# Kernel tuning notes

Hardware: AMD Instinct MI355X
Metric: run time of the kernel (lower is better)

## Reference

```python
import jax, jax.numpy as jnp
import numpy as np

N = 65536          # nodes
E = 1048576        # edges (avg degree 16)
K = 5              # B-spline kernel size per dim (dim=3 -> 125 kernels)
F_IN, F_OUT = 1, 32
GRID = 32          # first sparse_voxel_max_pool: size = 1/32 -> 32^3 voxels
NUM_VOX = GRID ** 3

# enumerate the 2^3 corners of the degree-1 B-spline support
_BITS = np.array([[(b >> d) & 1 for d in range(3)] for b in range(8)], dtype=np.int32)  # [8,3]
_STRIDES = np.array([1, K, K * K], dtype=np.int32)  # kernel index strides per dim


def setup_inputs() -> dict:
    key = jax.random.key(0)
    ks = jax.random.split(key, 7)
    x = jax.random.normal(ks[0], (N, F_IN), dtype=jnp.float32)
    edge_index = jax.random.randint(ks[1], (2, E), 0, N, dtype=jnp.int32)
    pseudo = jax.random.uniform(ks[2], (E, 3), dtype=jnp.float32)   # edge pseudo-coords in [0,1]^3
    pos = jax.random.uniform(ks[3], (N, 3), dtype=jnp.float32)      # node positions in [0,1]^3
    W = jax.random.normal(ks[4], (K ** 3, F_IN, F_OUT), dtype=jnp.float32) * 0.1
    W_root = jax.random.normal(ks[5], (F_IN, F_OUT), dtype=jnp.float32) * 0.1
    bias = jax.random.normal(ks[6], (F_OUT,), dtype=jnp.float32) * 0.1
    return {"x": x, "edge_index": edge_index, "pseudo": pseudo, "pos": pos,
            "W": W, "W_root": W_root, "bias": bias}


def spline_basis(pseudo):
    """Degree-1 open B-spline basis. Returns (weights [E,8], kernel_idx [E,8])."""
    v = pseudo * (K - 1)                                   # [E,3] in [0, K-1]
    i0 = jnp.clip(jnp.floor(v), 0, K - 2)                  # lower knot per dim
    f = v - i0                                             # fractional part
    i0 = i0.astype(jnp.int32)
    bits = jnp.asarray(_BITS)                              # [8,3]
    idx = i0[:, None, :] + bits[None]                      # [E,8,3]
    w = jnp.where(bits[None].astype(bool), f[:, None, :], 1.0 - f[:, None, :])
    B = w.prod(axis=-1)                                    # [E,8]
    kidx = (idx * jnp.asarray(_STRIDES)).sum(axis=-1)      # [E,8] in [0,125)
    return B, kidx


def spline_conv(x, edge_index, pseudo, W, W_root, bias):
    src, dst = edge_index[0], edge_index[1]
    B, kidx = spline_basis(pseudo)                         # [E,8], [E,8]
    xj = x[src]                                            # [E,F_IN] edge-wise gather
    Wg = W[kidx]                                           # [E,8,F_IN,F_OUT]
    msg = jnp.einsum('es,ef,esfo->eo', B, xj, Wg)          # basis-weighted messages [E,F_OUT]
    agg = jax.ops.segment_sum(msg, dst, num_segments=N)    # scatter-add
    deg = jax.ops.segment_sum(jnp.ones((E,), jnp.float32), dst, num_segments=N)
    out = agg / jnp.clip(deg, 1.0)[:, None] + x @ W_root + bias  # mean aggr + root + bias
    return out


def reference(x, edge_index, pseudo, pos, W, W_root, bias):
    h = jax.nn.elu(spline_conv(x, edge_index, pseudo, W, W_root, bias))  # [N,32]
    # sparse voxel max pooling: hash positions to a 32^3 grid, scatter-max features
    vid = jnp.clip(jnp.floor(pos * GRID), 0, GRID - 1).astype(jnp.int32)  # [N,3]
    vidx = vid[:, 0] + GRID * vid[:, 1] + GRID * GRID * vid[:, 2]         # [N]
    pooled = jax.ops.segment_max(h, vidx, num_segments=NUM_VOX)           # [32768,32]
    pooled = jnp.where(jnp.isfinite(pooled), pooled, 0.0)                 # empty voxels -> 0
    return pooled
```

## Files before the change

kernel.cpp:

```cpp
#include <hip/hip_runtime.h>
#include <math.h>

#define F_OUT     32
#define GRID_DIM  32
#define NUM_VOX   (GRID_DIM * GRID_DIM * GRID_DIM)

#define NPB   64
#define NBKT  1024
#define SEB   4096
#define SCS   127
#define FOCAP 2048

__device__ __forceinline__ unsigned int enc_f32(float f) {
    unsigned int u = __float_as_uint(f);
    return (u & 0x80000000u) ? ~u : (u | 0x80000000u);
}
__device__ __forceinline__ float dec_f32(unsigned int e) {
    return (e & 0x80000000u) ? __uint_as_float(e ^ 0x80000000u)
                             : __uint_as_float(~e);
}

__global__ __launch_bounds__(512) void sort_kernel(
    const int*   __restrict__ src,
    const int*   __restrict__ dst,
    const float* __restrict__ x,
    const float* __restrict__ pseudo,
    float4* __restrict__ payload,
    unsigned int* __restrict__ off_tab,
    int E)
{
    __shared__ unsigned int   sHist[NBKT];
    __shared__ unsigned int   sStart[NBKT];
    __shared__ unsigned int   sScan[512];
    __shared__ unsigned int   sPairE[SEB];
    __shared__ unsigned short sPairD[SEB];

    const int t   = threadIdx.x;
    const int blk = blockIdx.x;
    const int e0  = blk * SEB;

    for (int i = t; i < NBKT; i += 512) sHist[i] = 0;
    __syncthreads();

    unsigned short dloc[8];
    #pragma unroll
    for (int i = 0; i < 8; ++i) {
        int e = e0 + i * 512 + t;
        if (e < E) {
            int d = dst[e];
            dloc[i] = (unsigned short)d;
            atomicAdd(&sHist[d >> 6], 1u);
        } else dloc[i] = 0;
    }
    __syncthreads();

    unsigned int a0 = sHist[2 * t], a1 = sHist[2 * t + 1];
    sScan[t] = a0 + a1;
    __syncthreads();
    for (int ofs = 1; ofs < 512; ofs <<= 1) {
        unsigned int v = (t >= ofs) ? sScan[t - ofs] : 0u;
        __syncthreads();
        sScan[t] += v;
        __syncthreads();
    }
    unsigned int excl = sScan[t] - (a0 + a1);
    sStart[2 * t]     = excl;
    sStart[2 * t + 1] = excl + a0;
    __syncthreads();
    sHist[2 * t]     = excl;
    sHist[2 * t + 1] = excl + a0;
    __syncthreads();

    #pragma unroll
    for (int i = 0; i < 8; ++i) {
        int e = e0 + i * 512 + t;
        if (e < E) {
            unsigned int slot = atomicAdd(&sHist[dloc[i] >> 6], 1u);
            sPairE[slot] = (unsigned int)e;
            sPairD[slot] = dloc[i];
        }
    }
    __syncthreads();

    int total = E - e0; if (total > SEB) total = SEB;

    for (int i = t; i < total; i += 512) {
        unsigned int e = sPairE[i];
        unsigned int d = sPairD[i];
        float xj = x[src[e]];
        float p0 = pseudo[3 * e], p1 = pseudo[3 * e + 1], p2 = pseudo[3 * e + 2];
        unsigned int q2 = (unsigned int)(p2 * 65535.0f + 0.5f) & 0xFFFFu;
        unsigned int w  = q2 | ((d & 63u) << 16);
        payload[(size_t)e0 + i] = make_float4(p0, p1, xj, __uint_as_float(w));
    }

    for (int b = t; b < NBKT; b += 512)
        off_tab[(size_t)blk * (NBKT + 1) + b] = (unsigned int)e0 + sStart[b];
    if (t == 0)
        off_tab[(size_t)blk * (NBKT + 1) + NBKT] = (unsigned int)(e0 + total);
}

__global__ __launch_bounds__(512) void owner_kernel(
    const float4* __restrict__ payload,
    const unsigned int* __restrict__ off_tab,
    const float* __restrict__ W,
    const float* __restrict__ x,
    const float* __restrict__ W_root,
    const float* __restrict__ bias,
    const float* __restrict__ pos,
    unsigned int* __restrict__ pooled,
    int Nn, int nSB)
{
    __shared__ __align__(16) float sC[NPB * SCS];
    __shared__ unsigned int  sGS[256];
    __shared__ unsigned int  sLS[257];
    __shared__ unsigned int  sTmp[256];
    __shared__ unsigned char sFO[FOCAP];

    const int t = threadIdx.x;
    const int b = blockIdx.x;

    for (int i = t; i < NPB * SCS / 4; i += 512)
        *(float4*)&sC[i * 4] = make_float4(0.f, 0.f, 0.f, 0.f);

    unsigned int cnt = 0;
    if (t < 256) {
        if (t < nSB) {
            unsigned int s  = off_tab[(size_t)t * (NBKT + 1) + b];
            unsigned int e_ = off_tab[(size_t)t * (NBKT + 1) + b + 1];
            sGS[t] = s;
            cnt = e_ - s;
        } else sGS[t] = 0;
        sTmp[t] = cnt;
    }
    __syncthreads();
    for (int ofs = 1; ofs < 256; ofs <<= 1) {
        unsigned int v = 0;
        if (t < 256 && t >= ofs) v = sTmp[t - ofs];
        __syncthreads();
        if (t < 256) sTmp[t] += v;
        __syncthreads();
    }
    if (t < 256) sLS[t] = sTmp[t] - cnt;
    if (t == 255) sLS[256] = sTmp[255];
    __syncthreads();
    const int ne = (int)sLS[256];

    if (t < 256 && t < nSB) {
        unsigned int ls = sLS[t];
        for (unsigned int j = 0; j < cnt; ++j) {
            unsigned int idx = ls + j;
            if (idx < FOCAP) sFO[idx] = (unsigned char)t;
        }
    }
    __syncthreads();

    for (int i = t; i < ne; i += 512) {
        int f;
        if (i < FOCAP) f = sFO[i];
        else {
            int lo = 0, hi = 255;
            while (lo < hi) {
                int mid = (lo + hi + 1) >> 1;
                if (sLS[mid] <= (unsigned int)i) lo = mid; else hi = mid - 1;
            }
            f = lo;
        }
        unsigned int g = sGS[f] + ((unsigned int)i - sLS[f]);
        float4 r = payload[g];

        float xj = r.z;
        unsigned int w = __float_as_uint(r.w);
        int   rel = (int)((w >> 16) & 63u);
        float p2  = (float)(w & 0xFFFFu) * (1.0f / 65535.0f);

        float v0 = r.x * 4.0f, v1 = r.y * 4.0f, v2 = p2 * 4.0f;
        float i0 = fminf(fmaxf(floorf(v0), 0.0f), 3.0f);
        float i1 = fminf(fmaxf(floorf(v1), 0.0f), 3.0f);
        float i2 = fminf(fmaxf(floorf(v2), 0.0f), 3.0f);
        float f0 = v0 - i0, f1 = v1 - i1, f2 = v2 - i2;
        float g0 = 1.0f - f0, g1 = 1.0f - f1, g2 = 1.0f - f2;
        int k = (int)i0 + 5 * (int)i1 + 25 * (int)i2;

        float w00 = g0 * g1, w10 = f0 * g1, w01 = g0 * f1, w11 = f0 * f1;
        float a2 = xj * g2, b2 = xj * f2;
        float* row = sC + rel * SCS;
        atomicAdd(row + k +  0, w00 * a2);
        atomicAdd(row + k +  1, w10 * a2);
        atomicAdd(row + k +  5, w01 * a2);
        atomicAdd(row + k +  6, w11 * a2);
        atomicAdd(row + k + 25, w00 * b2);
        atomicAdd(row + k + 26, w10 * b2);
        atomicAdd(row + k + 30, w01 * b2);
        atomicAdd(row + k + 31, w11 * b2);
        atomicAdd(row + 125, 1.0f);
    }
    __syncthreads();

    const int node = t & 63;
    const int cg   = t >> 6;
    const float* crow = sC + node * SCS;
    float4 acc = make_float4(0.f, 0.f, 0.f, 0.f);
    #pragma unroll 5
    for (int k = 0; k < 125; ++k) {
        float r = crow[k];
        float4 wv = *(const float4*)(W + k * F_OUT + cg * 4);
        acc.x += r * wv.x; acc.y += r * wv.y;
        acc.z += r * wv.z; acc.w += r * wv.w;
    }
    float dg = fmaxf(crow[125], 1.0f);
    int   n  = b * NPB + node;
    float xn = (n < Nn) ? x[n] : 0.0f;
    float4 wr = *(const float4*)(W_root + cg * 4);
    float4 bs = *(const float4*)(bias + cg * 4);
    __syncthreads();

    if (n < Nn) {
        float h;
        h = acc.x / dg + xn * wr.x + bs.x; h = h > 0.f ? h : expm1f(h); sC[node * SCS + cg * 4 + 0] = h;
        h = acc.y / dg + xn * wr.y + bs.y; h = h > 0.f ? h : expm1f(h); sC[node * SCS + cg * 4 + 1] = h;
        h = acc.z / dg + xn * wr.z + bs.z; h = h > 0.f ? h : expm1f(h); sC[node * SCS + cg * 4 + 2] = h;
        h = acc.w / dg + xn * wr.w + bs.w; h = h > 0.f ? h : expm1f(h); sC[node * SCS + cg * 4 + 3] = h;
    }
    __syncthreads();

    for (int item = t; item < NPB * F_OUT; item += 512) {
        int nr = item >> 5, o = item & 31;
        int nn = b * NPB + nr;
        if (nn >= Nn) break;
        int vx = min(max((int)floorf(pos[3 * nn + 0] * (float)GRID_DIM), 0), GRID_DIM - 1);
        int vy = min(max((int)floorf(pos[3 * nn + 1] * (float)GRID_DIM), 0), GRID_DIM - 1);
        int vz = min(max((int)floorf(pos[3 * nn + 2] * (float)GRID_DIM), 0), GRID_DIM - 1);
        int vidx = vx + GRID_DIM * vy + GRID_DIM * GRID_DIM * vz;
        atomicMax(&pooled[(size_t)vidx * F_OUT + o], enc_f32(sC[nr * SCS + o]));
    }
}

__global__ __launch_bounds__(256) void finalize_kernel(
    const unsigned int* __restrict__ pooled,
    float* __restrict__ out, int M)
{
    int i = blockIdx.x * blockDim.x + threadIdx.x;
    if (i >= M) return;
    unsigned int u = pooled[i];
    out[i] = (u == 0u) ? 0.0f : dec_f32(u);
}

extern "C" void kernel_launch(void* const* d_in, const int* in_sizes, int n_in,
                              void* d_out, int out_size, void* d_ws, size_t ws_size,
                              hipStream_t stream) {
    const float* x       = (const float*)d_in[0];
    const int*   ei      = (const int*)  d_in[1];
    const float* pseudo  = (const float*)d_in[2];
    const float* pos     = (const float*)d_in[3];
    const float* W       = (const float*)d_in[4];
    const float* W_root  = (const float*)d_in[5];
    const float* bias    = (const float*)d_in[6];
    float* out = (float*)d_out;

    const int E   = in_sizes[1] / 2;
    const int Nn  = in_sizes[0];
    const int nSB = (E + SEB - 1) / SEB;
    const int nb  = (Nn + NPB - 1) / NPB;

    const size_t pooled_b = (size_t)NUM_VOX * F_OUT * 4;
    const size_t off_b    = (size_t)nSB * (NBKT + 1) * 4;
    unsigned int* pooled  = (unsigned int*)d_ws;
    unsigned int* off_tab = (unsigned int*)((char*)d_ws + pooled_b);
    float4*       payload = (float4*)((char*)d_ws + pooled_b + ((off_b + 15) & ~(size_t)15));

    hipMemsetAsync(pooled, 0, pooled_b, stream);

    sort_kernel<<<nSB, 512, 0, stream>>>(ei, ei + E, x, pseudo, payload, off_tab, E);
    owner_kernel<<<nb, 512, 0, stream>>>(payload, off_tab, W, x, W_root, bias, pos,
                                         pooled, Nn, nSB);

    const int M = (out_size < NUM_VOX * F_OUT) ? out_size : NUM_VOX * F_OUT;
    finalize_kernel<<<(M + 255) / 256, 256, 0, stream>>>(pooled, out, M);
}
```

Before: 173.3 us.

## Gather edge payload before bucketing and simplify owner-side edge indexing

The sort kernel now loads src, pseudo and x[src] in the first pass, before any sorting. It stages full float4 payloads in LDS and writes them out contiguously, which replaces the second scattered gather pass. The sort chunk size is halved so the LDS payload buffer fits. The offset table is packed as start|count per bucket. The owner kernel replaces its 256-wide block scan and segment lookup with a wave-shuffle scan plus an atomic base, building an LDS list of edge indices, with a direct-processing fallback when that list overflows. The W contraction is also vectorized over float4 rows. The trade-offs are twice as many sort blocks, twice as many segments per owner block, and a non-deterministic order of edge accumulation.

Result: faster. 167.3 us (-3.4%).

```diff
diff --git a/kernel.cpp b/kernel.cpp
--- a/kernel.cpp
+++ b/kernel.cpp
@@ -7,9 +7,10 @@
 
 #define NPB   64
 #define NBKT  1024
-#define SEB   4096
-#define SCS   127
-#define FOCAP 2048
+#define SEB   2048
+#define SCS   132
+#define DEGS  125
+#define ECAP  3072
 
 __device__ __forceinline__ unsigned int enc_f32(float f) {
     unsigned int u = __float_as_uint(f);
@@ -29,26 +30,31 @@
     unsigned int* __restrict__ off_tab,
     int E)
 {
-    __shared__ unsigned int   sHist[NBKT];
-    __shared__ unsigned int   sStart[NBKT];
-    __shared__ unsigned int   sScan[512];
-    __shared__ unsigned int   sPairE[SEB];
-    __shared__ unsigned short sPairD[SEB];
-
-    const int t   = threadIdx.x;
-    const int blk = blockIdx.x;
-    const int e0  = blk * SEB;
+    __shared__ unsigned int sHist[NBKT];
+    __shared__ unsigned int sStart[NBKT];
+    __shared__ unsigned int sScan[512];
+    __shared__ __align__(16) float4 sPay[SEB];
+
+    const int t  = threadIdx.x;
+    const int e0 = blockIdx.x * SEB;
 
     for (int i = t; i < NBKT; i += 512) sHist[i] = 0;
     __syncthreads();
 
-    unsigned short dloc[8];
+    unsigned short dloc[4];
+    float4 pay[4];
     #pragma unroll
-    for (int i = 0; i < 8; ++i) {
+    for (int i = 0; i < 4; ++i) {
         int e = e0 + i * 512 + t;
         if (e < E) {
             int d = dst[e];
+            int s = src[e];
+            float p0 = pseudo[3 * e], p1 = pseudo[3 * e + 1], p2 = pseudo[3 * e + 2];
+            float xj = x[s];
+            unsigned int q2 = (unsigned int)(p2 * 65535.0f + 0.5f) & 0xFFFFu;
+            unsigned int w  = q2 | ((unsigned int)(d & 63) << 16);
             dloc[i] = (unsigned short)d;
+            pay[i]  = make_float4(p0, p1, xj, __uint_as_float(w));
             atomicAdd(&sHist[d >> 6], 1u);
         } else dloc[i] = 0;
     }
@@ -70,34 +76,55 @@
     sHist[2 * t]     = excl;
     sHist[2 * t + 1] = excl + a0;
     __syncthreads();
+    const unsigned int total = sScan[511];
 
     #pragma unroll
-    for (int i = 0; i < 8; ++i) {
+    for (int i = 0; i < 4; ++i) {
         int e = e0 + i * 512 + t;
         if (e < E) {
             unsigned int slot = atomicAdd(&sHist[dloc[i] >> 6], 1u);
-            sPairE[slot] = (unsigned int)e;
-            sPairD[slot] = dloc[i];
+            sPay[slot] = pay[i];
         }
     }
     __syncthreads();
 
-    int total = E - e0; if (total > SEB) total = SEB;
-
-    for (int i = t; i < total; i += 512) {
-        unsigned int e = sPairE[i];
-        unsigned int d = sPairD[i];
-        float xj = x[src[e]];
-        float p0 = pseudo[3 * e], p1 = pseudo[3 * e + 1], p2 = pseudo[3 * e + 2];
-        unsigned int q2 = (unsigned int)(p2 * 65535.0f + 0.5f) & 0xFFFFu;
-        unsigned int w  = q2 | ((d & 63u) << 16);
-        payload[(size_t)e0 + i] = make_float4(p0, p1, xj, __uint_as_float(w));
-    }
-
-    for (int b = t; b < NBKT; b += 512)
-        off_tab[(size_t)blk * (NBKT + 1) + b] = (unsigned int)e0 + sStart[b];
-    if (t == 0)
-        off_tab[(size_t)blk * (NBKT + 1) + NBKT] = (unsigned int)(e0 + total);
+    for (unsigned int i = t; i < total; i += 512)
+        payload[(size_t)e0 + i] = sPay[i];
+
+    for (int b = t; b < NBKT; b += 512) {
+        unsigned int s = sStart[b];
+        unsigned int nxt = (b < NBKT - 1) ? sStart[b + 1] : total;
+        off_tab[(size_t)blockIdx.x * NBKT + b] = s | ((nxt - s) << 16);
+    }
+}
+
+__device__ __forceinline__ void process_edge(float4 r, float* sC)
+{
+    float xj = r.z;
+    unsigned int w = __float_as_uint(r.w);
+    int   rel = (int)((w >> 16) & 63u);
+    float p2  = (float)(w & 0xFFFFu) * (1.0f / 65535.0f);
+
+    float v0 = r.x * 4.0f, v1 = r.y * 4.0f, v2 = p2 * 4.0f;
+    float i0 = fminf(fmaxf(floorf(v0), 0.0f), 3.0f);
+    float i1 = fminf(fmaxf(floorf(v1), 0.0f), 3.0f);
+    float i2 = fminf(fmaxf(floorf(v2), 0.0f), 3.0f);
+    float f0 = v0 - i0, f1 = v1 - i1, f2 = v2 - i2;
+    float g0 = 1.0f - f0, g1 = 1.0f - f1, g2 = 1.0f - f2;
+    int k = (int)i0 + 5 * (int)i1 + 25 * (int)i2;
+
+    float w00 = g0 * g1, w10 = f0 * g1, w01 = g0 * f1, w11 = f0 * f1;
+    float a2 = xj * g2, b2 = xj * f2;
+    float* row = sC + rel * SCS;
+    atomicAdd(row + k +  0, w00 * a2);
+    atomicAdd(row + k +  1, w10 * a2);
+    atomicAdd(row + k +  5, w01 * a2);
+    atomicAdd(row + k +  6, w11 * a2);
+    atomicAdd(row + k + 25, w00 * b2);
+    atomicAdd(row + k + 26, w10 * b2);
+    atomicAdd(row + k + 30, w01 * b2);
+    atomicAdd(row + k + 31, w11 * b2);
+    atomicAdd(row + DEGS, 1.0f);
 }
 
 __global__ __launch_bounds__(512) void owner_kernel(
@@ -112,103 +139,73 @@
     int Nn, int nSB)
 {
     __shared__ __align__(16) float sC[NPB * SCS];
-    __shared__ unsigned int  sGS[256];
-    __shared__ unsigned int  sLS[257];
-    __shared__ unsigned int  sTmp[256];
-    __shared__ unsigned char sFO[FOCAP];
+    __shared__ unsigned int sEdge[ECAP];
+    __shared__ unsigned int sNe;
 
     const int t = threadIdx.x;
     const int b = blockIdx.x;
+    const int lane = t & 63;
 
     for (int i = t; i < NPB * SCS / 4; i += 512)
         *(float4*)&sC[i * 4] = make_float4(0.f, 0.f, 0.f, 0.f);
-
-    unsigned int cnt = 0;
-    if (t < 256) {
-        if (t < nSB) {
-            unsigned int s  = off_tab[(size_t)t * (NBKT + 1) + b];
-            unsigned int e_ = off_tab[(size_t)t * (NBKT + 1) + b + 1];
-            sGS[t] = s;
-            cnt = e_ - s;
-        } else sGS[t] = 0;
-        sTmp[t] = cnt;
-    }
-    __syncthreads();
-    for (int ofs = 1; ofs < 256; ofs <<= 1) {
-        unsigned int v = 0;
-        if (t < 256 && t >= ofs) v = sTmp[t - ofs];
-        __syncthreads();
-        if (t < 256) sTmp[t] += v;
-        __syncthreads();
-    }
-    if (t < 256) sLS[t] = sTmp[t] - cnt;
-    if (t == 255) sLS[256] = sTmp[255];
-    __syncthreads();
-    const int ne = (int)sLS[256];
-
-    if (t < 256 && t < nSB) {
-        unsigned int ls = sLS[t];
-        for (unsigned int j = 0; j < cnt; ++j) {
-            unsigned int idx = ls + j;
-            if (idx < FOCAP) sFO[idx] = (unsigned char)t;
-        }
-    }
-    __syncthreads();
-
-    for (int i = t; i < ne; i += 512) {
-        int f;
-        if (i < FOCAP) f = sFO[i];
-        else {
-            int lo = 0, hi = 255;
-            while (lo < hi) {
-                int mid = (lo + hi + 1) >> 1;
-                if (sLS[mid] <= (unsigned int)i) lo = mid; else hi = mid - 1;
-            }
-            f = lo;
-        }
-        unsigned int g = sGS[f] + ((unsigned int)i - sLS[f]);
-        float4 r = payload[g];
-
-        float xj = r.z;
-        unsigned int w = __float_as_uint(r.w);
-        int   rel = (int)((w >> 16) & 63u);
-        float p2  = (float)(w & 0xFFFFu) * (1.0f / 65535.0f);
-
-        float v0 = r.x * 4.0f, v1 = r.y * 4.0f, v2 = p2 * 4.0f;
-        float i0 = fminf(fmaxf(floorf(v0), 0.0f), 3.0f);
-        float i1 = fminf(fmaxf(floorf(v1), 0.0f), 3.0f);
-        float i2 = fminf(fmaxf(floorf(v2), 0.0f), 3.0f);
-        float f0 = v0 - i0, f1 = v1 - i1, f2 = v2 - i2;
-        float g0 = 1.0f - f0, g1 = 1.0f - f1, g2 = 1.0f - f2;
-        int k = (int)i0 + 5 * (int)i1 + 25 * (int)i2;
-
-        float w00 = g0 * g1, w10 = f0 * g1, w01 = g0 * f1, w11 = f0 * f1;
-        float a2 = xj * g2, b2 = xj * f2;
-        float* row = sC + rel * SCS;
-        atomicAdd(row + k +  0, w00 * a2);
-        atomicAdd(row + k +  1, w10 * a2);
-        atomicAdd(row + k +  5, w01 * a2);
-        atomicAdd(row + k +  6, w11 * a2);
-        atomicAdd(row + k + 25, w00 * b2);
-        atomicAdd(row + k + 26, w10 * b2);
-        atomicAdd(row + k + 30, w01 * b2);
-        atomicAdd(row + k + 31, w11 * b2);
-        atomicAdd(row + 125, 1.0f);
-    }
+    if (t == 0) sNe = 0;
+
+    unsigned int cnt = 0, start_g = 0;
+    if (t < nSB) {
+        unsigned int packed = off_tab[(size_t)t * NBKT + b];
+        start_g = (unsigned int)t * SEB + (packed & 0xFFFFu);
+        cnt = packed >> 16;
+    }
+    __syncthreads();
+
+    unsigned int incl = cnt;
+    #pragma unroll
+    for (int d = 1; d < 64; d <<= 1) {
+        unsigned int v = __shfl_up(incl, d, 64);
+        if (lane >= d) incl += v;
+    }
+    unsigned int wtot = __shfl(incl, 63, 64);
+    unsigned int wbase = 0;
+    if (lane == 63 && wtot > 0) wbase = atomicAdd(&sNe, wtot);
+    wbase = __shfl(wbase, 63, 64);
+    unsigned int off = wbase + incl - cnt;
+
+    for (unsigned int j = 0; j < cnt; ++j) {
+        unsigned int p = off + j;
+        if (p < ECAP) sEdge[p] = start_g + j;
+        else process_edge(payload[start_g + j], sC);
+    }
+    __syncthreads();
+
+    int ne = (int)sNe; if (ne > ECAP) ne = ECAP;
+    for (int i = t; i < ne; i += 512)
+        process_edge(payload[sEdge[i]], sC);
     __syncthreads();
 
     const int node = t & 63;
     const int cg   = t >> 6;
     const float* crow = sC + node * SCS;
     float4 acc = make_float4(0.f, 0.f, 0.f, 0.f);
-    #pragma unroll 5
-    for (int k = 0; k < 125; ++k) {
-        float r = crow[k];
-        float4 wv = *(const float4*)(W + k * F_OUT + cg * 4);
-        acc.x += r * wv.x; acc.y += r * wv.y;
-        acc.z += r * wv.z; acc.w += r * wv.w;
-    }
-    float dg = fmaxf(crow[125], 1.0f);
+    #pragma unroll 8
+    for (int k4 = 0; k4 < 31; ++k4) {
+        float4 r = *(const float4*)&crow[k4 * 4];
+        const float* wp = W + (k4 * 4) * F_OUT + cg * 4;
+        float4 w0 = *(const float4*)(wp);
+        float4 w1 = *(const float4*)(wp + F_OUT);
+        float4 w2 = *(const float4*)(wp + 2 * F_OUT);
+        float4 w3 = *(const float4*)(wp + 3 * F_OUT);
+        acc.x += r.x * w0.x + r.y * w1.x + r.z * w2.x + r.w * w3.x;
+        acc.y += r.x * w0.y + r.y * w1.y + r.z * w2.y + r.w * w3.y;
+        acc.z += r.x * w0.z + r.y * w1.z + r.z * w2.z + r.w * w3.z;
+        acc.w += r.x * w0.w + r.y * w1.w + r.z * w2.w + r.w * w3.w;
+    }
+    {
+        float r = crow[124];
+        const float* wp = W + 124 * F_OUT + cg * 4;
+        acc.x += r * wp[0]; acc.y += r * wp[1];
+        acc.z += r * wp[2]; acc.w += r * wp[3];
+    }
+    float dg = fmaxf(crow[DEGS], 1.0f);
     int   n  = b * NPB + node;
     float xn = (n < Nn) ? x[n] : 0.0f;
     float4 wr = *(const float4*)(W_root + cg * 4);
@@ -264,7 +261,7 @@
     const int nb  = (Nn + NPB - 1) / NPB;
 
     const size_t pooled_b = (size_t)NUM_VOX * F_OUT * 4;
-    const size_t off_b    = (size_t)nSB * (NBKT + 1) * 4;
+    const size_t off_b    = (size_t)nSB * NBKT * 4;
     unsigned int* pooled  = (unsigned int*)d_ws;
     unsigned int* off_tab = (unsigned int*)((char*)d_ws + pooled_b);
     float4*       payload = (float4*)((char*)d_ws + pooled_b + ((off_b + 15) & ~(size_t)15));
```
